# Optimization experiments

Measured on AMD Instinct MI355X. Metric: run time of the kernel, lower is better.

Reference implementation:

```python
import jax, jax.numpy as jnp
import numpy as np

QMIN, QMAX = 0.0, 255.0  # uint8 affine quantization range


def setup_inputs() -> dict:
    key = jax.random.key(0)
    ks = jax.random.split(key, 7)
    B, S, IN, OUT = 4, 2048, 4096, 4096
    x = jax.random.normal(ks[0], (B, S, IN), dtype=jnp.float32)
    weight_q = jax.random.randint(ks[1], (OUT, IN), 0, 255, dtype=jnp.int32)
    weight_scales = jax.random.uniform(ks[2], (OUT,), dtype=jnp.float32) * 0.01 + 1e-4
    weight_zero_points = jax.random.randint(ks[3], (OUT,), 0, 255, dtype=jnp.int32)
    act_scales = jax.random.uniform(ks[4], (1,), dtype=jnp.float32) * 0.05 + 1e-3
    act_zero_points = jnp.full((1,), 128, dtype=jnp.int32)
    bias = jax.random.normal(ks[5], (OUT,), dtype=jnp.float32)
    return {
        "x": x,
        "weight_q": weight_q,
        "weight_scales": weight_scales,
        "weight_zero_points": weight_zero_points,
        "act_scales": act_scales,
        "act_zero_points": act_zero_points,
        "bias": bias,
    }


def reference(x, weight_q, weight_scales, weight_zero_points, act_scales, act_zero_points, bias):
    # quantize_from_qparams on activations (per-tensor affine, uint8 range)
    a_zp = act_zero_points.astype(jnp.float32)
    x_q = jnp.clip(jnp.round(x / act_scales) + a_zp, QMIN, QMAX)
    # linear_on_quantized_data: dequantize both operands, fused matmul + bias
    x_deq = (x_q - a_zp) * act_scales  # [B, S, IN]
    w_deq = (weight_q.astype(jnp.float32) - weight_zero_points.astype(jnp.float32)[:, None]) \
            * weight_scales[:, None]  # [OUT, IN], per-output-channel scale/zp
    out = jnp.einsum("bsi,oi->bso", x_deq, w_deq) + bias  # [B, S, OUT]
    return out
```

## Files before the change

### kernel.cpp

```cpp
#include <hip/hip_runtime.h>
#include <hip/hip_bf16.h>

using int32x4 = __attribute__((ext_vector_type(4))) int;

#define BM 128
#define BN 128
#define BKQ 64

__device__ __forceinline__ void load_lds16(const void* g, void* l) {
    __builtin_amdgcn_global_load_lds(
        (const __attribute__((address_space(1))) unsigned int*)g,
        (__attribute__((address_space(3))) unsigned int*)l, 16, 0, 0);
}

__global__ __launch_bounds__(256) void quant_rows(
    const float* __restrict__ x, const float* __restrict__ act_scale,
    const int* __restrict__ act_zp, char* __restrict__ xs,
    int* __restrict__ rowsum, int K)
{
    __shared__ int wsum[4];
    const int row = blockIdx.x;
    const float s = act_scale[0];
    const int zp = act_zp[0];
    const float4* __restrict__ xr = (const float4*)(x + (size_t)row * K);
    char4* __restrict__ xo = (char4*)(xs + (size_t)row * K);
    const int nv = K >> 2;
    int sum = 0;
    for (int i = threadIdx.x; i < nv; i += 256) {
        float4 v = xr[i];
        int q0 = min(max((int)rintf(v.x / s) + zp, 0), 255) - zp;
        int q1 = min(max((int)rintf(v.y / s) + zp, 0), 255) - zp;
        int q2 = min(max((int)rintf(v.z / s) + zp, 0), 255) - zp;
        int q3 = min(max((int)rintf(v.w / s) + zp, 0), 255) - zp;
        sum += q0 + q1 + q2 + q3;
        char4 c;
        c.x = (char)q0; c.y = (char)q1; c.z = (char)q2; c.w = (char)q3;
        xo[i] = c;
    }
    for (int off = 32; off > 0; off >>= 1) sum += __shfl_down(sum, off, 64);
    if ((threadIdx.x & 63) == 0) wsum[threadIdx.x >> 6] = sum;
    __syncthreads();
    if (threadIdx.x == 0) rowsum[row] = wsum[0] + wsum[1] + wsum[2] + wsum[3];
}

__global__ __launch_bounds__(256) void wconv(
    const int4* __restrict__ wq, char4* __restrict__ wsq, long n4)
{
    long i = (long)blockIdx.x * 256 + threadIdx.x;
    if (i >= n4) return;
    int4 v = wq[i];
    char4 c;
    c.x = (char)(v.x - 128); c.y = (char)(v.y - 128);
    c.z = (char)(v.z - 128); c.w = (char)(v.w - 128);
    wsq[i] = c;
}

__global__ __launch_bounds__(256) void mkscales(
    const float* __restrict__ wscale, const int* __restrict__ wzp,
    const float* __restrict__ act_scale, float* __restrict__ alpha,
    float* __restrict__ beta, int N)
{
    int n = blockIdx.x * 256 + threadIdx.x;
    if (n >= N) return;
    float a = act_scale[0] * wscale[n];
    alpha[n] = a;
    beta[n] = a * (float)(128 - wzp[n]);
}

__global__ __launch_bounds__(256) void gemm_i8(
    const char* __restrict__ Aq, const char* __restrict__ Bq,
    const int* __restrict__ rowsum, const float* __restrict__ alpha,
    const float* __restrict__ beta, const float* __restrict__ bias,
    float* __restrict__ C, int M, int N, int K)
{
    __shared__ __align__(16) char As[BM * BKQ];
    __shared__ __align__(16) char Bs[BN * BKQ];

    const int tid  = threadIdx.x;
    const int wave = tid >> 6;
    const int lane = tid & 63;

    const int n0 = blockIdx.x * BN;
    const int m0 = blockIdx.y * BM;

    const int wm = (wave & 1) * 64;
    const int wn = (wave >> 1) * 64;

    const int cA  = wave * 128 + lane;
    const int cA2 = cA + 64;
    const char* aga = Aq + (size_t)(m0 + (cA  >> 2)) * K + (cA  & 3) * 16;
    const char* agb = Aq + (size_t)(m0 + (cA2 >> 2)) * K + (cA2 & 3) * 16;
    const char* bga = Bq + (size_t)(n0 + (cA  >> 2)) * K + (cA  & 3) * 16;
    const char* bgb = Bq + (size_t)(n0 + (cA2 >> 2)) * K + (cA2 & 3) * 16;
    char* lA0 = As + wave * 2048;
    char* lA1 = As + wave * 2048 + 1024;
    char* lB0 = Bs + wave * 2048;
    char* lB1 = Bs + wave * 2048 + 1024;

    int32x4 acc[4][4] = {};

    const int r = lane & 15;
    const int q = lane >> 4;

    for (int k0 = 0; k0 < K; k0 += BKQ) {
        __syncthreads();
        load_lds16(aga, lA0); aga += BKQ;
        load_lds16(agb, lA1); agb += BKQ;
        load_lds16(bga, lB0); bga += BKQ;
        load_lds16(bgb, lB1); bgb += BKQ;
        __syncthreads();

        int32x4 af[4], bf[4];
#pragma unroll
        for (int i = 0; i < 4; i++)
            af[i] = *(const int32x4*)(As + (wm + i * 16 + r) * 64 + q * 16);
#pragma unroll
        for (int j = 0; j < 4; j++)
            bf[j] = *(const int32x4*)(Bs + (wn + j * 16 + r) * 64 + q * 16);

#pragma unroll
        for (int i = 0; i < 4; i++)
#pragma unroll
            for (int j = 0; j < 4; j++)
                acc[i][j] = __builtin_amdgcn_mfma_i32_16x16x64_i8(
                    af[i], bf[j], acc[i][j], 0, 0, 0);
    }

    const int r4  = (lane >> 4) * 4;
    const int cil = lane & 15;
#pragma unroll
    for (int j = 0; j < 4; j++) {
        const int col = n0 + wn + j * 16 + cil;
        const float al = alpha[col];
        const float be = beta[col];
        const float bi = bias[col];
#pragma unroll
        for (int i = 0; i < 4; i++) {
            const int rowb = m0 + wm + i * 16 + r4;
#pragma unroll
            for (int t = 0; t < 4; t++) {
                const int row = rowb + t;
                C[(size_t)row * N + col] =
                    al * (float)acc[i][j][t] + be * (float)rowsum[row] + bi;
            }
        }
    }
}

extern "C" void kernel_launch(void* const* d_in, const int* in_sizes, int n_in,
                              void* d_out, int out_size, void* d_ws, size_t ws_size,
                              hipStream_t stream) {
    const float* x      = (const float*)d_in[0];
    const int*   wq     = (const int*)d_in[1];
    const float* wscale = (const float*)d_in[2];
    const int*   wzp    = (const int*)d_in[3];
    const float* ascale = (const float*)d_in[4];
    const int*   azp    = (const int*)d_in[5];
    const float* bias   = (const float*)d_in[6];
    float* out = (float*)d_out;

    const int N = in_sizes[2];
    const int K = in_sizes[1] / N;
    const int M = in_sizes[0] / K;

    char* ws     = (char*)d_ws;
    char* xs     = ws;
    char* wsq    = ws + (size_t)M * K;
    int*  rowsum = (int*)(wsq + (size_t)N * K);
    float* alpha = (float*)((char*)rowsum + (size_t)M * 4);
    float* beta  = (float*)((char*)alpha + (size_t)N * 4);

    quant_rows<<<M, 256, 0, stream>>>(x, ascale, azp, xs, rowsum, K);

    long n4 = (long)N * K / 4;
    wconv<<<(int)((n4 + 255) / 256), 256, 0, stream>>>(
        (const int4*)wq, (char4*)wsq, n4);

    mkscales<<<(N + 255) / 256, 256, 0, stream>>>(wscale, wzp, ascale, alpha, beta, N);

    dim3 grid(N / BN, M / BM);
    gemm_i8<<<grid, 256, 0, stream>>>(xs, wsq, rowsum, alpha, beta, bias, out, M, N, K);
}
```

Baseline: 478.3 us.

## Double K tile to 128 with XOR-swizzled LDS layout and occupancy hint

Raises the GEMM K-step from 64 to 128 bytes, which halves the number of barrier pairs per output tile. The global-to-LDS loads are reorganised so that each wave fills 8-row bands, and the 16-byte chunks within each 128-byte row are XOR-swizzled by row to avoid LDS bank conflicts on the fragment reads. It also adds a launch_bounds occupancy hint of 4 blocks per CU. LDS use doubles to 32KB per block, and the swizzle has to match exactly between the writes and the reads.

New measurement: 411.8 us. 13.9% less time.

```diff
diff --git a/kernel.cpp b/kernel.cpp
--- a/kernel.cpp
+++ b/kernel.cpp
@@ -5,7 +5,7 @@
 
 #define BM 128
 #define BN 128
-#define BKQ 64
+#define BKQ 128
 
 __device__ __forceinline__ void load_lds16(const void* g, void* l) {
     __builtin_amdgcn_global_load_lds(
@@ -67,7 +67,7 @@
     beta[n] = a * (float)(128 - wzp[n]);
 }
 
-__global__ __launch_bounds__(256) void gemm_i8(
+__global__ __launch_bounds__(256, 4) void gemm_i8(
     const char* __restrict__ Aq, const char* __restrict__ Bq,
     const int* __restrict__ rowsum, const float* __restrict__ alpha,
     const float* __restrict__ beta, const float* __restrict__ bias,
@@ -86,44 +86,50 @@
     const int wm = (wave & 1) * 64;
     const int wn = (wave >> 1) * 64;
 
-    const int cA  = wave * 128 + lane;
-    const int cA2 = cA + 64;
-    const char* aga = Aq + (size_t)(m0 + (cA  >> 2)) * K + (cA  & 3) * 16;
-    const char* agb = Aq + (size_t)(m0 + (cA2 >> 2)) * K + (cA2 & 3) * 16;
-    const char* bga = Bq + (size_t)(n0 + (cA  >> 2)) * K + (cA  & 3) * 16;
-    const char* bgb = Bq + (size_t)(n0 + (cA2 >> 2)) * K + (cA2 & 3) * 16;
-    char* lA0 = As + wave * 2048;
-    char* lA1 = As + wave * 2048 + 1024;
-    char* lB0 = Bs + wave * 2048;
-    char* lB1 = Bs + wave * 2048 + 1024;
+    const int srow = wave * 8 + (lane >> 3);
+    const int scol = ((lane & 7) ^ (lane >> 3)) * 16;
+    const char* ag = Aq + (size_t)(m0 + srow) * K + scol;
+    const char* bg = Bq + (size_t)(n0 + srow) * K + scol;
+    const size_t band = (size_t)32 * K;
+
+    char* lA = As + wave * 1024;
+    char* lB = Bs + wave * 1024;
 
     int32x4 acc[4][4] = {};
 
-    const int r = lane & 15;
-    const int q = lane >> 4;
+    const int r  = lane & 15;
+    const int q  = lane >> 4;
+    const int rx = r & 7;
 
     for (int k0 = 0; k0 < K; k0 += BKQ) {
         __syncthreads();
-        load_lds16(aga, lA0); aga += BKQ;
-        load_lds16(agb, lA1); agb += BKQ;
-        load_lds16(bga, lB0); bga += BKQ;
-        load_lds16(bgb, lB1); bgb += BKQ;
+#pragma unroll
+        for (int u = 0; u < 4; u++) {
+            load_lds16(ag + u * band, lA + u * 4096);
+            load_lds16(bg + u * band, lB + u * 4096);
+        }
+        ag += BKQ;
+        bg += BKQ;
         __syncthreads();
 
-        int32x4 af[4], bf[4];
 #pragma unroll
-        for (int i = 0; i < 4; i++)
-            af[i] = *(const int32x4*)(As + (wm + i * 16 + r) * 64 + q * 16);
+        for (int kb = 0; kb < 2; kb++) {
+            int32x4 af[4], bf[4];
 #pragma unroll
-        for (int j = 0; j < 4; j++)
-            bf[j] = *(const int32x4*)(Bs + (wn + j * 16 + r) * 64 + q * 16);
-
-#pragma unroll
-        for (int i = 0; i < 4; i++)
+            for (int i = 0; i < 4; i++)
+                af[i] = *(const int32x4*)(As + (wm + i * 16 + r) * 128
+                                             + (((kb * 4 + q) ^ rx) * 16));
 #pragma unroll
             for (int j = 0; j < 4; j++)
-                acc[i][j] = __builtin_amdgcn_mfma_i32_16x16x64_i8(
-                    af[i], bf[j], acc[i][j], 0, 0, 0);
+                bf[j] = *(const int32x4*)(Bs + (wn + j * 16 + r) * 128
+                                             + (((kb * 4 + q) ^ rx) * 16));
+#pragma unroll
+            for (int i = 0; i < 4; i++)
+#pragma unroll
+                for (int j = 0; j < 4; j++)
+                    acc[i][j] = __builtin_amdgcn_mfma_i32_16x16x64_i8(
+                        af[i], bf[j], acc[i][j], 0, 0, 0);
+        }
     }
 
     const int r4  = (lane >> 4) * 4;
```
